# Optimization experiments

Measured on AMD Instinct MI355X. Metric: run time of the kernel, lower is better.

Reference implementation:

```python
import jax, jax.numpy as jnp
import numpy as np

B, N, FA, FP, C = 64, 64, 75, 14, 128


def _mlp2(x, W0, b0, W1, b1):
    # two lazy-Linear + ReLU sub-layers (n_sub_layer=2)
    h = jax.nn.relu(x @ W0 + b0)
    return jax.nn.relu(h @ W1 + b1)


def setup_inputs() -> dict:
    key = jax.random.key(0)
    ks = jax.random.split(key, 32)
    w = lambda k, s: jax.random.normal(k, s, jnp.float32) * 0.05
    inp = {
        "atom_x": jax.random.normal(ks[0], (B, N, FA), jnp.float32),
        "pair_x": jax.random.normal(ks[1], (B, N * N, FP), jnp.float32),
        # atom_to_atom: FA -> C -> C
        "a2a_W0": w(ks[2], (FA, C)), "a2a_b0": w(ks[3], (C,)),
        "a2a_W1": w(ks[4], (C, C)), "a2a_b1": w(ks[5], (C,)),
        # pair_to_atom: FP -> C -> C
        "p2a_W0": w(ks[6], (FP, C)), "p2a_b0": w(ks[7], (C,)),
        "p2a_W1": w(ks[8], (C, C)), "p2a_b1": w(ks[9], (C,)),
        # atom_layer: 2C -> C -> C
        "al_W0": w(ks[10], (2 * C, C)), "al_b0": w(ks[11], (C,)),
        "al_W1": w(ks[12], (C, C)), "al_b1": w(ks[13], (C,)),
        # atom_to_pair (weights shared across both orderings): 2FA -> C -> C
        "a2p_W0": w(ks[14], (2 * FA, C)), "a2p_b0": w(ks[15], (C,)),
        "a2p_W1": w(ks[16], (C, C)), "a2p_b1": w(ks[17], (C,)),
        # pair_to_pair: FP -> C -> C
        "p2p_W0": w(ks[18], (FP, C)), "p2p_b0": w(ks[19], (C,)),
        "p2p_W1": w(ks[20], (C, C)), "p2p_b1": w(ks[21], (C,)),
        # pair_layer: 2C -> C -> C
        "pl_W0": w(ks[22], (2 * C, C)), "pl_b0": w(ks[23], (C,)),
        "pl_W1": w(ks[24], (C, C)), "pl_b1": w(ks[25], (C,)),
    }
    return inp


def reference(atom_x, pair_x,
              a2a_W0, a2a_b0, a2a_W1, a2a_b1,
              p2a_W0, p2a_b0, p2a_W1, p2a_b1,
              al_W0, al_b0, al_W1, al_b1,
              a2p_W0, a2p_b0, a2p_W1, a2p_b1,
              p2p_W0, p2p_b0, p2p_W1, p2p_b1,
              pl_W0, pl_b0, pl_W1, pl_b1):
    b, n, fa = atom_x.shape
    # --- atom branch ---
    a0 = _mlp2(atom_x, a2a_W0, a2a_b0, a2a_W1, a2a_b1)            # [B,N,C]
    a1 = _mlp2(pair_x, p2a_W0, p2a_b0, p2a_W1, p2a_b1)            # [B,N*N,C]
    a1 = a1.reshape(b, n, n, -1).sum(axis=2)                      # PairToAtom sum
    a = jnp.concatenate([a0, a1], axis=-1)                        # [B,N,2C]
    next_atom = jax.nn.relu(_mlp2(a, al_W0, al_b0, al_W1, al_b1))  # extra relu per forward
    # --- pair branch ---
    rep = jnp.broadcast_to(atom_x[:, None, :, :], (b, n, n, fa))  # atom_repeat
    til = jnp.broadcast_to(atom_x[:, :, None, :], (b, n, n, fa))  # atom_tile
    pr0 = jnp.concatenate([til, rep], axis=-1).reshape(b, n * n, 2 * fa)
    pr1 = jnp.concatenate([rep, til], axis=-1).reshape(b, n * n, 2 * fa)
    p0 = (_mlp2(pr0, a2p_W0, a2p_b0, a2p_W1, a2p_b1)
          + _mlp2(pr1, a2p_W0, a2p_b0, a2p_W1, a2p_b1))            # [B,N*N,C]
    p1 = _mlp2(pair_x, p2p_W0, p2p_b0, p2p_W1, p2p_b1)            # [B,N*N,C]
    p = jnp.concatenate([p0, p1], axis=-1)                        # [B,N*N,2C]
    next_pair = jax.nn.relu(_mlp2(p, pl_W0, pl_b0, pl_W1, pl_b1))
    return (next_atom, next_pair)
```

## Files before the change

### kernel.cpp

```cpp
#include <hip/hip_runtime.h>
#include <hip/hip_bf16.h>

typedef unsigned short u16;
typedef unsigned int u32;
typedef __attribute__((ext_vector_type(8))) __bf16 bf16x8;
typedef __attribute__((ext_vector_type(4))) float f32x4;

#define B_ 64
#define N_ 64
#define FA_ 75
#define FP_ 14
#define C_ 128

__device__ float g_A0[4096 * 128];
__device__ float g_A1[4096 * 128];
__device__ float g_TB[4096 * 256];
__device__ u16   g_Wf[208896];
__device__ int   g_isbf;

#define OFF_AA0   0
#define OFF_AA1   12288
#define OFF_APT   28672
#define OFF_APB   40960
#define OFF_PA0   53248
#define OFF_PA1   57344
#define OFF_AL0   73728
#define OFF_AL1   106496
#define OFF_AP1   122880
#define OFF_PP0   139264
#define OFF_PP1   143360
#define OFF_PL0T  159744
#define OFF_PL0B  176128
#define OFF_PL1   192512

__device__ __forceinline__ float bf2f(u16 a) {
    union { u32 u; float f; } v; v.u = ((u32)a) << 16; return v.f;
}
__device__ __forceinline__ u16 f2bf(float f) {
    union { float f; u32 u; } v; v.f = f;
    u32 r = v.u + 0x7fffu + ((v.u >> 16) & 1u);
    return (u16)(r >> 16);
}
#if __has_builtin(__builtin_amdgcn_cvt_pk_bf16_f32)
__device__ __forceinline__ u32 f2bf_pk(float a, float b) {
    auto r = __builtin_amdgcn_cvt_pk_bf16_f32(a, b);
    if constexpr (sizeof(r) == 4) {
        union { decltype(r) v; u32 u; } c; c.v = r; return c.u;
    } else {
        return (u32)f2bf(a) | ((u32)f2bf(b) << 16);
    }
}
#else
__device__ __forceinline__ u32 f2bf_pk(float a, float b) {
    return (u32)f2bf(a) | ((u32)f2bf(b) << 16);
}
#endif

__device__ __forceinline__ u16 ldw(const void* p, size_t i, bool isbf) {
    if (isbf) return ((const u16*)p)[i];
    return f2bf(((const float*)p)[i]);
}
__device__ __forceinline__ float ldf(const void* p, size_t i, bool isbf) {
    if (isbf) return bf2f(((const u16*)p)[i]);
    return ((const float*)p)[i];
}
__device__ __forceinline__ f32x4 ldf4(const void* p, int i, bool isbf) {
    f32x4 r;
    if (isbf) {
        const u16* q = (const u16*)p + i;
        r[0] = bf2f(q[0]); r[1] = bf2f(q[1]); r[2] = bf2f(q[2]); r[3] = bf2f(q[3]);
    } else {
        r = *(const f32x4*)((const float*)p + i);
    }
    return r;
}
__device__ __forceinline__ uint4 pack8(const void* p, size_t base, int kmax, int k0, bool isbf) {
    uint4 u;
    if (isbf) {
        const u16* q = (const u16*)p + base;
        u16 h[8];
#pragma unroll
        for (int j = 0; j < 8; ++j) h[j] = (k0 + j < kmax) ? q[k0 + j] : (u16)0;
        u.x = (u32)h[0] | ((u32)h[1] << 16); u.y = (u32)h[2] | ((u32)h[3] << 16);
        u.z = (u32)h[4] | ((u32)h[5] << 16); u.w = (u32)h[6] | ((u32)h[7] << 16);
    } else {
        const float* q = (const float*)p + base;
        float f[8];
#pragma unroll
        for (int j = 0; j < 8; ++j) f[j] = (k0 + j < kmax) ? q[k0 + j] : 0.f;
        u.x = f2bf_pk(f[0], f[1]); u.y = f2bf_pk(f[2], f[3]);
        u.z = f2bf_pk(f[4], f[5]); u.w = f2bf_pk(f[6], f[7]);
    }
    return u;
}

__global__ void detect_k(const void* __restrict__ atom) {
    if (threadIdx.x == 0) {
        const u32* a = (const u32*)atom;
        int sane = 0;
        for (int w = 0; w < 64; ++w) {
            u32 ex = (a[w] >> 7) & 0xffu;
            sane += (ex >= 113u && ex <= 133u) ? 1 : 0;
        }
        g_isbf = (sane >= 32) ? 1 : 0;
    }
}

__global__ __launch_bounds__(256) void prep_w(
    const void* aaW0, const void* aaW1, const void* apW0,
    const void* paW0, const void* paW1, const void* alW0, const void* alW1,
    const void* apW1, const void* ppW0, const void* ppW1,
    const void* plW0, const void* plW1) {
    const void* srcs[14] = {aaW0, aaW1, apW0, apW0, paW0, paW1, alW0, alW1,
                            apW1, ppW0, ppW1, plW0, plW0, plW1};
    const int Ktab[14]  = {75, 128, 75, 75, 14, 128, 256, 128, 128, 14, 128, 128, 128, 128};
    const int KStab[14] = {3, 4, 3, 3, 1, 4, 8, 4, 4, 1, 4, 4, 4, 4};
    const int rofft[14] = {0, 0, 0, 75, 0, 0, 0, 0, 0, 0, 0, 0, 128, 0};
    const int baset[14] = {OFF_AA0, OFF_AA1, OFF_APT, OFF_APB, OFF_PA0, OFF_PA1,
                           OFF_AL0, OFF_AL1, OFF_AP1, OFF_PP0, OFF_PP1,
                           OFF_PL0T, OFF_PL0B, OFF_PL1};
    int gid = blockIdx.x * 256 + threadIdx.x;
    int j = 0, s = gid;
    while (j < 14 && s >= KStab[j] * 512) { s -= KStab[j] * 512; ++j; }
    if (j >= 14) return;
    const bool isbf = g_isbf != 0;
    int lane = s & 63, rest = s >> 6;
    int ks = rest % KStab[j], mt = rest / KStab[j];
    int m = mt * 16 + (lane & 15), q = lane >> 4;
    float f[8];
#pragma unroll
    for (int jj = 0; jj < 8; ++jj) {
        int k = ks * 32 + q * 8 + jj;
        f[jj] = (k < Ktab[j]) ? ldf(srcs[j], (size_t)(rofft[j] + k) * 128 + m, isbf) : 0.f;
    }
    uint4 u;
    u.x = f2bf_pk(f[0], f[1]); u.y = f2bf_pk(f[2], f[3]);
    u.z = f2bf_pk(f[4], f[5]); u.w = f2bf_pk(f[6], f[7]);
    *(uint4*)&g_Wf[(size_t)baset[j] + (size_t)s * 8] = u;
}

template<int KS, int NT>
__device__ __forceinline__ void gemm2(const u16* __restrict__ wf,
                                      const u16* __restrict__ bF,
                                      int mt0, int lane, f32x4 (&acc)[2][NT]) {
#pragma unroll
    for (int ks = 0; ks < KS; ++ks) {
        bf16x8 a0 = *(const bf16x8*)(wf + (((mt0    ) * KS + ks) * 64 + lane) * 8);
        bf16x8 a1 = *(const bf16x8*)(wf + (((mt0 + 1) * KS + ks) * 64 + lane) * 8);
#pragma unroll
        for (int nt = 0; nt < NT; ++nt) {
            bf16x8 b = *(const bf16x8*)(bF + ((nt * KS + ks) * 64 + lane) * 8);
            acc[0][nt] = __builtin_amdgcn_mfma_f32_16x16x32_bf16(a0, b, acc[0][nt], 0, 0, 0);
            acc[1][nt] = __builtin_amdgcn_mfma_f32_16x16x32_bf16(a1, b, acc[1][nt], 0, 0, 0);
        }
    }
}

__device__ __forceinline__ void frag_store(u16* dstF, int KSd, int nt, int mt, int lane, f32x4 v) {
    int c = lane & 15, quad = lane >> 4;
    int lp = c + 16 * ((2 * mt + (quad >> 1)) & 3);
    int ks = mt >> 1;
    uint2 u; u.x = f2bf_pk(v[0], v[1]); u.y = f2bf_pk(v[2], v[3]);
    *(uint2*)(dstF + (((nt * KSd + ks) * 64 + lp) * 8 + (quad & 1) * 4)) = u;
}

__device__ __forceinline__ void store_out4(void* outp, size_t elem, f32x4 v, bool isbf) {
    if (isbf) {
        uint2 u; u.x = f2bf_pk(v[0], v[1]); u.y = f2bf_pk(v[2], v[3]);
        *(uint2*)((u16*)outp + elem) = u;
    } else {
        *(f32x4*)((float*)outp + elem) = v;
    }
}

#define EPI_RELU_STORE(ACC, BB0, BB1, DST, NTN) do {                             \
    _Pragma("unroll") for (int ii = 0; ii < 2; ++ii) {                           \
        f32x4 bb_ = ii ? (BB1) : (BB0);                                          \
        _Pragma("unroll") for (int nt_ = 0; nt_ < NTN; ++nt_) {                  \
            f32x4 v_;                                                            \
            _Pragma("unroll") for (int r_ = 0; r_ < 4; ++r_) {                   \
                float x_ = ACC[ii][nt_][r_] + bb_[r_];                           \
                v_[r_] = x_ > 0.f ? x_ : 0.f;                                    \
            }                                                                    \
            frag_store(DST, 4, nt_, mt0 + ii, lane, v_);                         \
        }                                                                        \
    }                                                                            \
} while (0)

__global__ __launch_bounds__(256) void atom_pre(
    const void* __restrict__ atom,
    const void* __restrict__ aaB0, const void* __restrict__ aaB1) {
    __shared__ __align__(16) u16 sXF[2 * 3 * 64 * 8];
    __shared__ __align__(16) u16 sHF[2 * 4 * 64 * 8];
    const bool isbf = g_isbf != 0;
    const int t = threadIdx.x, lane = t & 63, w = t >> 6;
    const int quad = lane >> 4;
    const int r0g = blockIdx.x * 32;
    for (int s = t; s < 2 * 3 * 64; s += 256) {
        int lane_s = s & 63, rest = s >> 6;
        int ks = rest % 3, nt = rest / 3;
        int n = nt * 16 + (lane_s & 15), q = lane_s >> 4;
        *(uint4*)&sXF[s * 8] = pack8(atom, (size_t)(r0g + n) * FA_, FA_, ks * 32 + q * 8, isbf);
    }
    __syncthreads();
    const int mt0 = 2 * w;
    {
        f32x4 bb0 = ldf4(aaB0, mt0 * 16 + quad * 4, isbf);
        f32x4 bb1 = ldf4(aaB0, (mt0 + 1) * 16 + quad * 4, isbf);
        f32x4 acc[2][2];
#pragma unroll
        for (int ii = 0; ii < 2; ++ii)
#pragma unroll
            for (int nt = 0; nt < 2; ++nt) acc[ii][nt] = (f32x4){0.f, 0.f, 0.f, 0.f};
        gemm2<3, 2>(g_Wf + OFF_AA0, sXF, mt0, lane, acc);
        EPI_RELU_STORE(acc, bb0, bb1, sHF, 2);
    }
    __syncthreads();
    {
        f32x4 bb0 = ldf4(aaB1, mt0 * 16 + quad * 4, isbf);
        f32x4 bb1 = ldf4(aaB1, (mt0 + 1) * 16 + quad * 4, isbf);
        f32x4 acc[2][2];
#pragma unroll
        for (int ii = 0; ii < 2; ++ii)
#pragma unroll
            for (int nt = 0; nt < 2; ++nt) acc[ii][nt] = (f32x4){0.f, 0.f, 0.f, 0.f};
        gemm2<4, 2>(g_Wf + OFF_AA1, sHF, mt0, lane, acc);
        int c = lane & 15;
#pragma unroll
        for (int ii = 0; ii < 2; ++ii) {
            int mt = mt0 + ii;
            f32x4 bb = ii ? bb1 : bb0;
#pragma unroll
            for (int nt = 0; nt < 2; ++nt) {
                f32x4 v;
#pragma unroll
                for (int r = 0; r < 4; ++r) { float x = acc[ii][nt][r] + bb[r]; v[r] = x > 0.f ? x : 0.f; }
                *(f32x4*)&g_A0[(size_t)(r0g + nt * 16 + c) * 128 + mt * 16 + quad * 4] = v;
            }
        }
    }
    {
        f32x4 accT[2][2], accB[2][2];
#pragma unroll
        for (int ii = 0; ii < 2; ++ii)
#pragma unroll
            for (int nt = 0; nt < 2; ++nt) { accT[ii][nt] = (f32x4){0.f,0.f,0.f,0.f}; accB[ii][nt] = (f32x4){0.f,0.f,0.f,0.f}; }
        gemm2<3, 2>(g_Wf + OFF_APT, sXF, mt0, lane, accT);
        gemm2<3, 2>(g_Wf + OFF_APB, sXF, mt0, lane, accB);
        int c = lane & 15;
#pragma unroll
        for (int ii = 0; ii < 2; ++ii) {
            int mt = mt0 + ii;
#pragma unroll
            for (int nt = 0; nt < 2; ++nt) {
                size_t row = (size_t)(r0g + nt * 16 + c);
                *(f32x4*)&g_TB[row * 256 + mt * 16 + quad * 4] = accT[ii][nt];
                *(f32x4*)&g_TB[row * 256 + 128 + mt * 16 + quad * 4] = accB[ii][nt];
            }
        }
    }
}

__global__ __launch_bounds__(256) void p2a_sum(
    const void* __restrict__ pairx,
    const void* __restrict__ paB0, const void* __restrict__ paB1) {
    __shared__ __align__(16) u16 sPF[4 * 1 * 64 * 8];
    __shared__ __align__(16) u16 sHF[4 * 4 * 64 * 8];
    const bool isbf = g_isbf != 0;
    const int t = threadIdx.x, lane = t & 63, w = t >> 6;
    const int quad = lane >> 4;
    const int bx = blockIdx.x;
    const size_t rbase = (size_t)bx * 64;
    {
        int lane_s = t & 63, nt = t >> 6;
        int n = nt * 16 + (lane_s & 15), q = lane_s >> 4;
        *(uint4*)&sPF[t * 8] = pack8(pairx, (rbase + n) * FP_, FP_, q * 8, isbf);
    }
    __syncthreads();
    const int mt0 = 2 * w;
    {
        f32x4 bb0 = ldf4(paB0, mt0 * 16 + quad * 4, isbf);
        f32x4 bb1 = ldf4(paB0, (mt0 + 1) * 16 + quad * 4, isbf);
        f32x4 acc[2][4];
#pragma unroll
        for (int ii = 0; ii < 2; ++ii)
#pragma unroll
            for (int nt = 0; nt < 4; ++nt) acc[ii][nt] = (f32x4){0.f, 0.f, 0.f, 0.f};
        gemm2<1, 4>(g_Wf + OFF_PA0, sPF, mt0, lane, acc);
        EPI_RELU_STORE(acc, bb0, bb1, sHF, 4);
    }
    __syncthreads();
    {
        f32x4 bb0 = ldf4(paB1, mt0 * 16 + quad * 4, isbf);
        f32x4 bb1 = ldf4(paB1, (mt0 + 1) * 16 + quad * 4, isbf);
        f32x4 acc[2][4];
#pragma unroll
        for (int ii = 0; ii < 2; ++ii)
#pragma unroll
            for (int nt = 0; nt < 4; ++nt) acc[ii][nt] = (f32x4){0.f, 0.f, 0.f, 0.f};
        gemm2<4, 4>(g_Wf + OFF_PA1, sHF, mt0, lane, acc);
#pragma unroll
        for (int ii = 0; ii < 2; ++ii) {
            int mt = mt0 + ii;
            f32x4 bb = ii ? bb1 : bb0;
            f32x4 ssum = (f32x4){0.f, 0.f, 0.f, 0.f};
#pragma unroll
            for (int nt = 0; nt < 4; ++nt)
#pragma unroll
                for (int r = 0; r < 4; ++r) {
                    float x = acc[ii][nt][r] + bb[r];
                    ssum[r] += (x > 0.f ? x : 0.f);
                }
#pragma unroll
            for (int m = 1; m < 16; m <<= 1)
#pragma unroll
                for (int r = 0; r < 4; ++r) ssum[r] += __shfl_xor(ssum[r], m, 64);
            if ((lane & 15) == 0)
                *(f32x4*)&g_A1[(size_t)bx * 128 + mt * 16 + quad * 4] = ssum;
        }
    }
}

__global__ __launch_bounds__(256) void atom_layer(
    const void* __restrict__ alB0, const void* __restrict__ alB1,
    void* __restrict__ out) {
    __shared__ __align__(16) u16 sXF[1 * 8 * 64 * 8];
    __shared__ __align__(16) u16 sHF[1 * 4 * 64 * 8];
    const bool isbf = g_isbf != 0;
    const int t = threadIdx.x, lane = t & 63, w = t >> 6;
    const int quad = lane >> 4;
    const int r0g = blockIdx.x * 16;
    for (int s = t; s < 8 * 64; s += 256) {
        int lane_s = s & 63, ks = s >> 6;
        int n = lane_s & 15, q = lane_s >> 4;
        int k0 = ks * 32 + q * 8;
        const float* src = (k0 < 128) ? &g_A0[(size_t)(r0g + n) * 128 + k0]
                                      : &g_A1[(size_t)(r0g + n) * 128 + (k0 - 128)];
        f32x4 f0 = *(const f32x4*)src, f1 = *(const f32x4*)(src + 4);
        uint4 u;
        u.x = f2bf_pk(f0[0], f0[1]); u.y = f2bf_pk(f0[2], f0[3]);
        u.z = f2bf_pk(f1[0], f1[1]); u.w = f2bf_pk(f1[2], f1[3]);
        *(uint4*)&sXF[s * 8] = u;
    }
    __syncthreads();
    const int mt0 = 2 * w;
    {
        f32x4 bb0 = ldf4(alB0, mt0 * 16 + quad * 4, isbf);
        f32x4 bb1 = ldf4(alB0, (mt0 + 1) * 16 + quad * 4, isbf);
        f32x4 acc[2][1];
#pragma unroll
        for (int ii = 0; ii < 2; ++ii) acc[ii][0] = (f32x4){0.f, 0.f, 0.f, 0.f};
        gemm2<8, 1>(g_Wf + OFF_AL0, sXF, mt0, lane, acc);
        EPI_RELU_STORE(acc, bb0, bb1, sHF, 1);
    }
    __syncthreads();
    {
        f32x4 bb0 = ldf4(alB1, mt0 * 16 + quad * 4, isbf);
        f32x4 bb1 = ldf4(alB1, (mt0 + 1) * 16 + quad * 4, isbf);
        f32x4 acc[2][1];
#pragma unroll
        for (int ii = 0; ii < 2; ++ii) acc[ii][0] = (f32x4){0.f, 0.f, 0.f, 0.f};
        gemm2<4, 1>(g_Wf + OFF_AL1, sHF, mt0, lane, acc);
        int c = lane & 15;
#pragma unroll
        for (int ii = 0; ii < 2; ++ii) {
            int mt = mt0 + ii;
            f32x4 bb = ii ? bb1 : bb0;
            f32x4 v;
#pragma unroll
            for (int r = 0; r < 4; ++r) { float x = acc[ii][0][r] + bb[r]; v[r] = x > 0.f ? x : 0.f; }
            store_out4(out, (size_t)(r0g + c) * 128 + mt * 16 + quad * 4, v, isbf);
        }
    }
}

__global__ __launch_bounds__(256, 3) void pair_fused(
    const void* __restrict__ pairx,
    const void* __restrict__ apB0, const void* __restrict__ apB1,
    const void* __restrict__ ppB0, const void* __restrict__ ppB1,
    const void* __restrict__ plB0, const void* __restrict__ plB1,
    void* __restrict__ out) {
    __shared__ __align__(16) u16 sX1[4 * 4 * 64 * 8];
    __shared__ __align__(16) u16 sX2[4 * 4 * 64 * 8];
    __shared__ __align__(16) u16 sR [4 * 4 * 64 * 8];
    __shared__ __align__(16) u16 sPr[4 * 1 * 64 * 8];
    const bool isbf = g_isbf != 0;
    const int t = threadIdx.x, lane = t & 63, w = t >> 6;
    const int quad = lane >> 4, c = lane & 15;
    const int bx = blockIdx.x;
    const int b = bx >> 6, i = bx & 63;
    const int trow = b * 64;
    const size_t prow0 = (size_t)b * 4096 + (size_t)i * 64;
    const int mt0 = 2 * w;

    {
        int lane_s = t & 63, nt = t >> 6;
        int n = nt * 16 + (lane_s & 15), q = lane_s >> 4;
        *(uint4*)&sPr[t * 8] = pack8(pairx, (prow0 + n) * FP_, FP_, q * 8, isbf);
    }
    {
        const int ksg = t >> 6;
        const int k0 = ksg * 32 + quad * 8;
        const int rc = c;
        const float* TBi = &g_TB[(size_t)(trow + i) * 256 + k0];
        f32x4 t0 = *(const f32x4*)TBi,        t1 = *(const f32x4*)(TBi + 4);
        f32x4 o0 = *(const f32x4*)(TBi + 128), o1 = *(const f32x4*)(TBi + 132);
        f32x4 b0a = ldf4(apB0, k0, isbf), b0b = ldf4(apB0, k0 + 4, isbf);
        float Tip[8], Bip[8];
#pragma unroll
        for (int r = 0; r < 4; ++r) {
            Tip[r] = t0[r] + b0a[r]; Tip[4 + r] = t1[r] + b0b[r];
            Bip[r] = o0[r] + b0a[r]; Bip[4 + r] = o1[r] + b0b[r];
        }
#pragma unroll
        for (int nt = 0; nt < 4; ++nt) {
            int n = nt * 16 + rc;
            const float* Bj = &g_TB[(size_t)(trow + n) * 256 + k0];
            f32x4 j0 = *(const f32x4*)Bj,        j1 = *(const f32x4*)(Bj + 4);
            f32x4 j2 = *(const f32x4*)(Bj + 128), j3 = *(const f32x4*)(Bj + 132);
            float v0[8], v1[8];
#pragma unroll
            for (int r = 0; r < 4; ++r) {
                float x0 = Tip[r] + j2[r];      v0[r]     = x0 > 0.f ? x0 : 0.f;
                float x1 = Tip[4 + r] + j3[r];  v0[4 + r] = x1 > 0.f ? x1 : 0.f;
                float y0 = j0[r] + Bip[r];      v1[r]     = y0 > 0.f ? y0 : 0.f;
                float y1 = j1[r] + Bip[4 + r];  v1[4 + r] = y1 > 0.f ? y1 : 0.f;
            }
            uint4 u0, u1;
            u0.x = f2bf_pk(v0[0], v0[1]); u0.y = f2bf_pk(v0[2], v0[3]);
            u0.z = f2bf_pk(v0[4], v0[5]); u0.w = f2bf_pk(v0[6], v0[7]);
            u1.x = f2bf_pk(v1[0], v1[1]); u1.y = f2bf_pk(v1[2], v1[3]);
            u1.z = f2bf_pk(v1[4], v1[5]); u1.w = f2bf_pk(v1[6], v1[7]);
            int slot = ((nt * 4 + ksg) * 64 + lane) * 8;
            *(uint4*)&sX1[slot] = u0;
            *(uint4*)&sX2[slot] = u1;
        }
    }
    __syncthreads();
    f32x4 aH[2][4];
#pragma unroll
    for (int ii = 0; ii < 2; ++ii)
#pragma unroll
        for (int nt = 0; nt < 4; ++nt) aH[ii][nt] = (f32x4){0.f, 0.f, 0.f, 0.f};
    gemm2<1, 4>(g_Wf + OFF_PP0, sPr, mt0, lane, aH);
    {
        f32x4 bb0 = ldf4(apB1, mt0 * 16 + quad * 4, isbf);
        f32x4 bb1 = ldf4(apB1, (mt0 + 1) * 16 + quad * 4, isbf);
        f32x4 aA[2][4], aB[2][4];
#pragma unroll
        for (int ii = 0; ii < 2; ++ii)
#pragma unroll
            for (int nt = 0; nt < 4; ++nt) { aA[ii][nt] = (f32x4){0.f,0.f,0.f,0.f}; aB[ii][nt] = (f32x4){0.f,0.f,0.f,0.f}; }
        gemm2<4, 4>(g_Wf + OFF_AP1, sX1, mt0, lane, aA);
        gemm2<4, 4>(g_Wf + OFF_AP1, sX2, mt0, lane, aB);
#pragma unroll
        for (int ii = 0; ii < 2; ++ii) {
            int mt = mt0 + ii;
            f32x4 bb = ii ? bb1 : bb0;
#pragma unroll
            for (int nt = 0; nt < 4; ++nt) {
                f32x4 v;
#pragma unroll
                for (int r = 0; r < 4; ++r) {
                    float x = aA[ii][nt][r] + bb[r];
                    float y = aB[ii][nt][r] + bb[r];
                    v[r] = (x > 0.f ? x : 0.f) + (y > 0.f ? y : 0.f);
                }
                frag_store(sR, 4, nt, mt, lane, v);
            }
        }
    }
    __syncthreads();
    f32x4 C3[2][4];
#pragma unroll
    for (int ii = 0; ii < 2; ++ii)
#pragma unroll
        for (int nt = 0; nt < 4; ++nt) C3[ii][nt] = (f32x4){0.f, 0.f, 0.f, 0.f};
    gemm2<4, 4>(g_Wf + OFF_PL0T, sR, mt0, lane, C3);
    {
        f32x4 bb0 = ldf4(ppB0, mt0 * 16 + quad * 4, isbf);
        f32x4 bb1 = ldf4(ppB0, (mt0 + 1) * 16 + quad * 4, isbf);
        EPI_RELU_STORE(aH, bb0, bb1, sX1, 4);
    }
    __syncthreads();
    {
        f32x4 bb0 = ldf4(ppB1, mt0 * 16 + quad * 4, isbf);
        f32x4 bb1 = ldf4(ppB1, (mt0 + 1) * 16 + quad * 4, isbf);
        f32x4 aP[2][4];
#pragma unroll
        for (int ii = 0; ii < 2; ++ii)
#pragma unroll
            for (int nt = 0; nt < 4; ++nt) aP[ii][nt] = (f32x4){0.f, 0.f, 0.f, 0.f};
        gemm2<4, 4>(g_Wf + OFF_PP1, sX1, mt0, lane, aP);
        EPI_RELU_STORE(aP, bb0, bb1, sX2, 4);
    }
    __syncthreads();
    gemm2<4, 4>(g_Wf + OFF_PL0B, sX2, mt0, lane, C3);
    {
        f32x4 bb0 = ldf4(plB0, mt0 * 16 + quad * 4, isbf);
        f32x4 bb1 = ldf4(plB0, (mt0 + 1) * 16 + quad * 4, isbf);
        EPI_RELU_STORE(C3, bb0, bb1, sX1, 4);
    }
    __syncthreads();
    {
        f32x4 bb0 = ldf4(plB1, mt0 * 16 + quad * 4, isbf);
        f32x4 bb1 = ldf4(plB1, (mt0 + 1) * 16 + quad * 4, isbf);
        f32x4 aO[2][4];
#pragma unroll
        for (int ii = 0; ii < 2; ++ii)
#pragma unroll
            for (int nt = 0; nt < 4; ++nt) aO[ii][nt] = (f32x4){0.f, 0.f, 0.f, 0.f};
        gemm2<4, 4>(g_Wf + OFF_PL1, sX1, mt0, lane, aO);
        const size_t NA = (size_t)B_ * N_ * C_;
#pragma unroll
        for (int ii = 0; ii < 2; ++ii) {
            int mt = mt0 + ii;
            f32x4 bb = ii ? bb1 : bb0;
#pragma unroll
            for (int nt = 0; nt < 4; ++nt) {
                f32x4 v;
#pragma unroll
                for (int r = 0; r < 4; ++r) { float x = aO[ii][nt][r] + bb[r]; v[r] = x > 0.f ? x : 0.f; }
                store_out4(out, NA + (prow0 + nt * 16 + c) * 128 + mt * 16 + quad * 4, v, isbf);
            }
        }
    }
}

extern "C" void kernel_launch(void* const* d_in, const int* in_sizes, int n_in,
                              void* d_out, int out_size, void* d_ws, size_t ws_size,
                              hipStream_t stream) {
    const void* atom  = d_in[0];
    const void* pairx = d_in[1];
    const void* aaW0 = d_in[2];  const void* aaB0 = d_in[3];
    const void* aaW1 = d_in[4];  const void* aaB1 = d_in[5];
    const void* paW0 = d_in[6];  const void* paB0 = d_in[7];
    const void* paW1 = d_in[8];  const void* paB1 = d_in[9];
    const void* alW0 = d_in[10]; const void* alB0 = d_in[11];
    const void* alW1 = d_in[12]; const void* alB1 = d_in[13];
    const void* apW0 = d_in[14]; const void* apB0 = d_in[15];
    const void* apW1 = d_in[16]; const void* apB1 = d_in[17];
    const void* ppW0 = d_in[18]; const void* ppB0 = d_in[19];
    const void* ppW1 = d_in[20]; const void* ppB1 = d_in[21];
    const void* plW0 = d_in[22]; const void* plB0 = d_in[23];
    const void* plW1 = d_in[24]; const void* plB1 = d_in[25];
    (void)d_ws; (void)ws_size; (void)in_sizes; (void)n_in; (void)out_size;

    detect_k<<<1, 64, 0, stream>>>(atom);
    prep_w<<<102, 256, 0, stream>>>(aaW0, aaW1, apW0, paW0, paW1, alW0, alW1,
                                    apW1, ppW0, ppW1, plW0, plW1);
    atom_pre<<<128, 256, 0, stream>>>(atom, aaB0, aaB1);
    p2a_sum<<<4096, 256, 0, stream>>>(pairx, paB0, paB1);
    atom_layer<<<256, 256, 0, stream>>>(alB0, alB1, d_out);
    pair_fused<<<4096, 256, 0, stream>>>(pairx, apB0, apB1, ppB0, ppB1,
                                         plB0, plB1, d_out);
}
```

Before: 308.0 us.

## Fuse pair-to-atom MLP and sum into pair kernel; inline dtype detection

The separate p2a_sum kernel is removed. Its two-layer MLP and row-sum now run inside pair_fused, which reuses the pair_x tile already staged in shared memory, so pair_x is read from global memory once instead of twice. atom_layer is launched after pair_fused because it depends on the g_A1 sums. The detect_k launch is replaced by an in-kernel ballot over the first 64 words of atom_x, which saves a launch but repeats that small read in every block. The fused kernel holds more accumulators live, which may raise register pressure under its launch bound of 3.

```diff
diff --git a/kernel.cpp b/kernel.cpp
--- a/kernel.cpp
+++ b/kernel.cpp
@@ -16,7 +16,6 @@
 __device__ float g_A1[4096 * 128];
 __device__ float g_TB[4096 * 256];
 __device__ u16   g_Wf[208896];
-__device__ int   g_isbf;
 
 #define OFF_AA0   0
 #define OFF_AA1   12288
@@ -56,10 +55,13 @@
 }
 #endif
 
-__device__ __forceinline__ u16 ldw(const void* p, size_t i, bool isbf) {
-    if (isbf) return ((const u16*)p)[i];
-    return f2bf(((const float*)p)[i]);
-}
+__device__ __forceinline__ bool detect_isbf(const void* __restrict__ atom) {
+    u32 wrd = ((const u32*)atom)[threadIdx.x & 63];
+    u32 ex = (wrd >> 7) & 0xffu;
+    unsigned long long m = __ballot(ex >= 113u && ex <= 133u);
+    return __popcll(m) >= 32;
+}
+
 __device__ __forceinline__ float ldf(const void* p, size_t i, bool isbf) {
     if (isbf) return bf2f(((const u16*)p)[i]);
     return ((const float*)p)[i];
@@ -94,23 +96,13 @@
     return u;
 }
 
-__global__ void detect_k(const void* __restrict__ atom) {
-    if (threadIdx.x == 0) {
-        const u32* a = (const u32*)atom;
-        int sane = 0;
-        for (int w = 0; w < 64; ++w) {
-            u32 ex = (a[w] >> 7) & 0xffu;
-            sane += (ex >= 113u && ex <= 133u) ? 1 : 0;
-        }
-        g_isbf = (sane >= 32) ? 1 : 0;
-    }
-}
-
 __global__ __launch_bounds__(256) void prep_w(
+    const void* atom,
     const void* aaW0, const void* aaW1, const void* apW0,
     const void* paW0, const void* paW1, const void* alW0, const void* alW1,
     const void* apW1, const void* ppW0, const void* ppW1,
     const void* plW0, const void* plW1) {
+    const bool isbf = detect_isbf(atom);
     const void* srcs[14] = {aaW0, aaW1, apW0, apW0, paW0, paW1, alW0, alW1,
                             apW1, ppW0, ppW1, plW0, plW0, plW1};
     const int Ktab[14]  = {75, 128, 75, 75, 14, 128, 256, 128, 128, 14, 128, 128, 128, 128};
@@ -123,7 +115,6 @@
     int j = 0, s = gid;
     while (j < 14 && s >= KStab[j] * 512) { s -= KStab[j] * 512; ++j; }
     if (j >= 14) return;
-    const bool isbf = g_isbf != 0;
     int lane = s & 63, rest = s >> 6;
     int ks = rest % KStab[j], mt = rest / KStab[j];
     int m = mt * 16 + (lane & 15), q = lane >> 4;
@@ -192,7 +183,7 @@
     const void* __restrict__ aaB0, const void* __restrict__ aaB1) {
     __shared__ __align__(16) u16 sXF[2 * 3 * 64 * 8];
     __shared__ __align__(16) u16 sHF[2 * 4 * 64 * 8];
-    const bool isbf = g_isbf != 0;
+    const bool isbf = detect_isbf(atom);
     const int t = threadIdx.x, lane = t & 63, w = t >> 6;
     const int quad = lane >> 4;
     const int r0g = blockIdx.x * 32;
@@ -261,72 +252,13 @@
     }
 }
 
-__global__ __launch_bounds__(256) void p2a_sum(
-    const void* __restrict__ pairx,
-    const void* __restrict__ paB0, const void* __restrict__ paB1) {
-    __shared__ __align__(16) u16 sPF[4 * 1 * 64 * 8];
-    __shared__ __align__(16) u16 sHF[4 * 4 * 64 * 8];
-    const bool isbf = g_isbf != 0;
-    const int t = threadIdx.x, lane = t & 63, w = t >> 6;
-    const int quad = lane >> 4;
-    const int bx = blockIdx.x;
-    const size_t rbase = (size_t)bx * 64;
-    {
-        int lane_s = t & 63, nt = t >> 6;
-        int n = nt * 16 + (lane_s & 15), q = lane_s >> 4;
-        *(uint4*)&sPF[t * 8] = pack8(pairx, (rbase + n) * FP_, FP_, q * 8, isbf);
-    }
-    __syncthreads();
-    const int mt0 = 2 * w;
-    {
-        f32x4 bb0 = ldf4(paB0, mt0 * 16 + quad * 4, isbf);
-        f32x4 bb1 = ldf4(paB0, (mt0 + 1) * 16 + quad * 4, isbf);
-        f32x4 acc[2][4];
-#pragma unroll
-        for (int ii = 0; ii < 2; ++ii)
-#pragma unroll
-            for (int nt = 0; nt < 4; ++nt) acc[ii][nt] = (f32x4){0.f, 0.f, 0.f, 0.f};
-        gemm2<1, 4>(g_Wf + OFF_PA0, sPF, mt0, lane, acc);
-        EPI_RELU_STORE(acc, bb0, bb1, sHF, 4);
-    }
-    __syncthreads();
-    {
-        f32x4 bb0 = ldf4(paB1, mt0 * 16 + quad * 4, isbf);
-        f32x4 bb1 = ldf4(paB1, (mt0 + 1) * 16 + quad * 4, isbf);
-        f32x4 acc[2][4];
-#pragma unroll
-        for (int ii = 0; ii < 2; ++ii)
-#pragma unroll
-            for (int nt = 0; nt < 4; ++nt) acc[ii][nt] = (f32x4){0.f, 0.f, 0.f, 0.f};
-        gemm2<4, 4>(g_Wf + OFF_PA1, sHF, mt0, lane, acc);
-#pragma unroll
-        for (int ii = 0; ii < 2; ++ii) {
-            int mt = mt0 + ii;
-            f32x4 bb = ii ? bb1 : bb0;
-            f32x4 ssum = (f32x4){0.f, 0.f, 0.f, 0.f};
-#pragma unroll
-            for (int nt = 0; nt < 4; ++nt)
-#pragma unroll
-                for (int r = 0; r < 4; ++r) {
-                    float x = acc[ii][nt][r] + bb[r];
-                    ssum[r] += (x > 0.f ? x : 0.f);
-                }
-#pragma unroll
-            for (int m = 1; m < 16; m <<= 1)
-#pragma unroll
-                for (int r = 0; r < 4; ++r) ssum[r] += __shfl_xor(ssum[r], m, 64);
-            if ((lane & 15) == 0)
-                *(f32x4*)&g_A1[(size_t)bx * 128 + mt * 16 + quad * 4] = ssum;
-        }
-    }
-}
-
 __global__ __launch_bounds__(256) void atom_layer(
+    const void* __restrict__ atom,
     const void* __restrict__ alB0, const void* __restrict__ alB1,
     void* __restrict__ out) {
     __shared__ __align__(16) u16 sXF[1 * 8 * 64 * 8];
     __shared__ __align__(16) u16 sHF[1 * 4 * 64 * 8];
-    const bool isbf = g_isbf != 0;
+    const bool isbf = detect_isbf(atom);
     const int t = threadIdx.x, lane = t & 63, w = t >> 6;
     const int quad = lane >> 4;
     const int r0g = blockIdx.x * 16;
@@ -375,16 +307,18 @@
 }
 
 __global__ __launch_bounds__(256, 3) void pair_fused(
+    const void* __restrict__ atom,
     const void* __restrict__ pairx,
     const void* __restrict__ apB0, const void* __restrict__ apB1,
     const void* __restrict__ ppB0, const void* __restrict__ ppB1,
     const void* __restrict__ plB0, const void* __restrict__ plB1,
+    const void* __restrict__ paB0, const void* __restrict__ paB1,
     void* __restrict__ out) {
     __shared__ __align__(16) u16 sX1[4 * 4 * 64 * 8];
     __shared__ __align__(16) u16 sX2[4 * 4 * 64 * 8];
     __shared__ __align__(16) u16 sR [4 * 4 * 64 * 8];
     __shared__ __align__(16) u16 sPr[4 * 1 * 64 * 8];
-    const bool isbf = g_isbf != 0;
+    const bool isbf = detect_isbf(atom);
     const int t = threadIdx.x, lane = t & 63, w = t >> 6;
     const int quad = lane >> 4, c = lane & 15;
     const int bx = blockIdx.x;
@@ -437,12 +371,6 @@
         }
     }
     __syncthreads();
-    f32x4 aH[2][4];
-#pragma unroll
-    for (int ii = 0; ii < 2; ++ii)
-#pragma unroll
-        for (int nt = 0; nt < 4; ++nt) aH[ii][nt] = (f32x4){0.f, 0.f, 0.f, 0.f};
-    gemm2<1, 4>(g_Wf + OFF_PP0, sPr, mt0, lane, aH);
     {
         f32x4 bb0 = ldf4(apB1, mt0 * 16 + quad * 4, isbf);
         f32x4 bb1 = ldf4(apB1, (mt0 + 1) * 16 + quad * 4, isbf);
@@ -470,6 +398,13 @@
             }
         }
     }
+    f32x4 aH[2][4], aPA[2][4];
+#pragma unroll
+    for (int ii = 0; ii < 2; ++ii)
+#pragma unroll
+        for (int nt = 0; nt < 4; ++nt) { aH[ii][nt] = (f32x4){0.f,0.f,0.f,0.f}; aPA[ii][nt] = (f32x4){0.f,0.f,0.f,0.f}; }
+    gemm2<1, 4>(g_Wf + OFF_PP0, sPr, mt0, lane, aH);
+    gemm2<1, 4>(g_Wf + OFF_PA0, sPr, mt0, lane, aPA);
     __syncthreads();
     f32x4 C3[2][4];
 #pragma unroll
@@ -482,20 +417,49 @@
         f32x4 bb1 = ldf4(ppB0, (mt0 + 1) * 16 + quad * 4, isbf);
         EPI_RELU_STORE(aH, bb0, bb1, sX1, 4);
     }
-    __syncthreads();
-    {
+    {
+        f32x4 bb0 = ldf4(paB0, mt0 * 16 + quad * 4, isbf);
+        f32x4 bb1 = ldf4(paB0, (mt0 + 1) * 16 + quad * 4, isbf);
+        EPI_RELU_STORE(aPA, bb0, bb1, sX2, 4);
+    }
+    __syncthreads();
+    {
+        f32x4 aP[2][4], aA1[2][4];
+#pragma unroll
+        for (int ii = 0; ii < 2; ++ii)
+#pragma unroll
+            for (int nt = 0; nt < 4; ++nt) { aP[ii][nt] = (f32x4){0.f,0.f,0.f,0.f}; aA1[ii][nt] = (f32x4){0.f,0.f,0.f,0.f}; }
+        gemm2<4, 4>(g_Wf + OFF_PP1, sX1, mt0, lane, aP);
+        gemm2<4, 4>(g_Wf + OFF_PA1, sX2, mt0, lane, aA1);
+        {
+            f32x4 pb0 = ldf4(paB1, mt0 * 16 + quad * 4, isbf);
+            f32x4 pb1 = ldf4(paB1, (mt0 + 1) * 16 + quad * 4, isbf);
+#pragma unroll
+            for (int ii = 0; ii < 2; ++ii) {
+                int mt = mt0 + ii;
+                f32x4 bb = ii ? pb1 : pb0;
+                f32x4 ssum = (f32x4){0.f, 0.f, 0.f, 0.f};
+#pragma unroll
+                for (int nt = 0; nt < 4; ++nt)
+#pragma unroll
+                    for (int r = 0; r < 4; ++r) {
+                        float x = aA1[ii][nt][r] + bb[r];
+                        ssum[r] += (x > 0.f ? x : 0.f);
+                    }
+#pragma unroll
+                for (int m = 1; m < 16; m <<= 1)
+#pragma unroll
+                    for (int r = 0; r < 4; ++r) ssum[r] += __shfl_xor(ssum[r], m, 64);
+                if ((lane & 15) == 0)
+                    *(f32x4*)&g_A1[(size_t)bx * 128 + mt * 16 + quad * 4] = ssum;
+            }
+        }
         f32x4 bb0 = ldf4(ppB1, mt0 * 16 + quad * 4, isbf);
         f32x4 bb1 = ldf4(ppB1, (mt0 + 1) * 16 + quad * 4, isbf);
-        f32x4 aP[2][4];
-#pragma unroll
-        for (int ii = 0; ii < 2; ++ii)
-#pragma unroll
-            for (int nt = 0; nt < 4; ++nt) aP[ii][nt] = (f32x4){0.f, 0.f, 0.f, 0.f};
-        gemm2<4, 4>(g_Wf + OFF_PP1, sX1, mt0, lane, aP);
-        EPI_RELU_STORE(aP, bb0, bb1, sX2, 4);
-    }
-    __syncthreads();
-    gemm2<4, 4>(g_Wf + OFF_PL0B, sX2, mt0, lane, C3);
+        EPI_RELU_STORE(aP, bb0, bb1, sR, 4);
+    }
+    __syncthreads();
+    gemm2<4, 4>(g_Wf + OFF_PL0B, sR, mt0, lane, C3);
     {
         f32x4 bb0 = ldf4(plB0, mt0 * 16 + quad * 4, isbf);
         f32x4 bb1 = ldf4(plB0, (mt0 + 1) * 16 + quad * 4, isbf);
@@ -546,12 +510,10 @@
     const void* plW1 = d_in[24]; const void* plB1 = d_in[25];
     (void)d_ws; (void)ws_size; (void)in_sizes; (void)n_in; (void)out_size;
 
-    detect_k<<<1, 64, 0, stream>>>(atom);
-    prep_w<<<102, 256, 0, stream>>>(aaW0, aaW1, apW0, paW0, paW1, alW0, alW1,
+    prep_w<<<102, 256, 0, stream>>>(atom, aaW0, aaW1, apW0, paW0, paW1, alW0, alW1,
                                     apW1, ppW0, ppW1, plW0, plW1);
     atom_pre<<<128, 256, 0, stream>>>(atom, aaB0, aaB1);
-    p2a_sum<<<4096, 256, 0, stream>>>(pairx, paB0, paB1);
-    atom_layer<<<256, 256, 0, stream>>>(alB0, alB1, d_out);
-    pair_fused<<<4096, 256, 0, stream>>>(pairx, apB0, apB1, ppB0, ppB1,
-                                         plB0, plB1, d_out);
-}
+    pair_fused<<<4096, 256, 0, stream>>>(atom, pairx, apB0, apB1, ppB0, ppB1,
+                                         plB0, plB1, paB0, paB1, d_out);
+    atom_layer<<<256, 256, 0, stream>>>(atom, alB0, alB1, d_out);
+}
```

New measurement: 299.6 us. 2.7% less time.
